# Optimization experiments

Hardware: AMD Instinct MI355X
Metric: run time of the kernel (lower is better)

## Reference

```python
import jax, jax.numpy as jnp
import numpy as np

B, N, C = 128, 2048, 3
VL, PN = 256, 128  # vector_length, prediction_num
NEG_SLOPE = 0.01   # torch LeakyReLU default
BN_EPS = 1e-5


def _lin(key, fin, fout):
    k1, k2 = jax.random.split(key)
    lim = 1.0 / np.sqrt(fin)
    W = jax.random.uniform(k1, (fin, fout), minval=-lim, maxval=lim, dtype=jnp.float32)
    b = jax.random.uniform(k2, (fout,), minval=-lim, maxval=lim, dtype=jnp.float32)
    return W, b


def setup_inputs() -> dict:
    key = jax.random.key(0)
    ks = jax.random.split(key, 14)
    x = jax.random.normal(ks[0], (B, N, C), dtype=jnp.float32)
    lengths = jnp.maximum(jax.random.randint(ks[1], (B,), 0, N), 1).astype(jnp.int32)
    eps = jax.random.normal(ks[2], (B, VL), dtype=jnp.float32)
    W1, b1 = _lin(ks[3], C, 64)
    W2, b2 = _lin(ks[4], 64, 64)
    W3, b3 = _lin(ks[5], 64, 128)
    W4, b4 = _lin(ks[6], 128, 1024)
    Wf, bf = _lin(ks[7], 1024, 1024)
    Wmu, bmu = _lin(ks[8], 1024, VL)
    Wlv, blv = _lin(ks[9], 1024, VL)
    Wd1, bd1 = _lin(ks[10], VL, 1024)
    Wd2, bd2 = _lin(ks[11], 1024, 1024)
    Wd3, bd3 = _lin(ks[12], 1024, PN * C)
    g1 = jnp.ones((1024,), jnp.float32); be1 = jnp.zeros((1024,), jnp.float32)
    g2 = jnp.ones((1024,), jnp.float32); be2 = jnp.zeros((1024,), jnp.float32)
    return dict(x=x, lengths=lengths, eps=eps,
                W1=W1, b1=b1, W2=W2, b2=b2, W3=W3, b3=b3, W4=W4, b4=b4,
                Wf=Wf, bf=bf, Wmu=Wmu, bmu=bmu, Wlv=Wlv, blv=blv,
                Wd1=Wd1, bd1=bd1, g1=g1, be1=be1,
                Wd2=Wd2, bd2=bd2, g2=g2, be2=be2,
                Wd3=Wd3, bd3=bd3)


def _lrelu(h):
    return jnp.where(h > 0, h, NEG_SLOPE * h)


def _bn(h, g, b):
    # BatchNorm1d in training mode: biased batch stats
    m = h.mean(axis=0)
    v = h.var(axis=0)
    return (h - m) * jax.lax.rsqrt(v + BN_EPS) * g + b


def reference(x, lengths, eps,
              W1, b1, W2, b2, W3, b3, W4, b4,
              Wf, bf, Wmu, bmu, Wlv, blv,
              Wd1, bd1, g1, be1, Wd2, bd2, g2, be2, Wd3, bd3):
    # --- pointnet per-point MLP (batched over padded [B,N,C]) ---
    h = _lrelu(x @ W1 + b1)          # [B,N,64]
    h = _lrelu(h @ W2 + b2)          # [B,N,64]
    h = _lrelu(h @ W3 + b3)          # [B,N,128]
    h = _lrelu(h @ W4 + b4)          # [B,N,1024]
    # masked max over points (ragged -> padded+mask)
    mask = jnp.arange(N)[None, :] < lengths[:, None]   # [B,N]
    h = jnp.where(mask[:, :, None], h, -jnp.inf)
    pooled = jnp.max(h, axis=1)      # [B,1024]
    # --- encoder head ---
    e = _lrelu(pooled @ Wf + bf)
    mu = e @ Wmu + bmu               # [B,VL]
    logvar = e @ Wlv + blv           # [B,VL]
    # --- reparameterize ---
    z = mu + eps * jnp.exp(0.5 * logvar)
    # --- decoder: Linear+BN+LeakyReLU x2, final Linear ---
    d = _lrelu(_bn(z @ Wd1 + bd1, g1, be1))
    d = _lrelu(_bn(d @ Wd2 + bd2, g2, be2))
    y = (d @ Wd3 + bd3).reshape(-1, PN, C)   # [B,PN,C]
    return (y, mu, logvar)
```

## Files before the change

kernel.cpp:

```cpp
#include <hip/hip_runtime.h>
#include <hip/hip_bf16.h>
#include <math.h>

#define NEG_SLOPE 0.01f

typedef short short8 __attribute__((ext_vector_type(8)));
typedef float f32x4 __attribute__((ext_vector_type(4)));

__device__ __forceinline__ float lrelu(float v) { return v > 0.0f ? v : NEG_SLOPE * v; }

__device__ __forceinline__ short f2bf(float f) {
    __hip_bfloat16 h = __float2bfloat16(f);
    return __builtin_bit_cast(short, h);
}

__global__ __launch_bounds__(256) void pack_all(
    const float* __restrict__ W4, const float* __restrict__ Wf,
    const float* __restrict__ Wmu, const float* __restrict__ Wlv,
    const float* __restrict__ Wd1, const float* __restrict__ Wd2,
    const float* __restrict__ Wd3, const float* __restrict__ W2,
    const float* __restrict__ W3,
    short* __restrict__ F4, short* __restrict__ Ff, short* __restrict__ Fmuvl,
    short* __restrict__ Fd1, short* __restrict__ Fd2, short* __restrict__ Fd3,
    short* __restrict__ F2, short* __restrict__ F3)
{
    int bid = blockIdx.x;
    const float* src = nullptr; short* dst = nullptr; int K = 0, N = 0; int muvl = 0;
    if      (bid < 64)   { src = W4;  dst = F4;    K = 128;  N = 1024; }
    else if (bid < 576)  { src = Wf;  dst = Ff;    K = 1024; N = 1024; bid -= 64; }
    else if (bid < 832)  { src = nullptr; dst = Fmuvl; K = 1024; N = 512; muvl = 1; bid -= 576; }
    else if (bid < 960)  { src = Wd1; dst = Fd1;   K = 256;  N = 1024; bid -= 832; }
    else if (bid < 1472) { src = Wd2; dst = Fd2;   K = 1024; N = 1024; bid -= 960; }
    else if (bid < 1664) { src = Wd3; dst = Fd3;   K = 1024; N = 384;  bid -= 1472; }
    else if (bid < 1666) { src = W2;  dst = F2;    K = 64;   N = 64;   bid -= 1664; }
    else                 { src = W3;  dst = F3;    K = 64;   N = 128;  bid -= 1666; }

    const int fragid = bid * 4 + (threadIdx.x >> 6);
    const int lane   = threadIdx.x & 63;
    const int K32    = K >> 5;
    const int t   = fragid / (K32 * 4);
    const int rem = fragid - t * K32 * 4;
    const int ks  = rem >> 2;
    const int n   = rem & 3;
    const int col   = t * 64 + n * 16 + (lane & 15);
    const int kbase = ks * 32 + (lane >> 4) * 8;

    short8 v;
#pragma unroll
    for (int e = 0; e < 8; ++e) {
        float f;
        if (muvl) f = (col < 256) ? Wmu[(size_t)(kbase + e) * 256 + col]
                                  : Wlv[(size_t)(kbase + e) * 256 + col - 256];
        else      f = src[(size_t)(kbase + e) * N + col];
        v[e] = f2bf(f);
    }
    *(short8*)&dst[(size_t)fragid * 512 + lane * 8] = v;
}

__global__ __launch_bounds__(128, 2) void h3_kernel(
    const float* __restrict__ x, const int* __restrict__ lengths,
    const float* __restrict__ W1, const float* __restrict__ b1,
    const float* __restrict__ b2, const float* __restrict__ b3,
    const short* __restrict__ F2, const short* __restrict__ F3,
    short* __restrict__ h3p)
{
    const int tid  = threadIdx.x;
    const int b    = blockIdx.x & 127;
    const int c2   = blockIdx.x >> 7;
    const int lane = tid & 63;
    const int w    = tid >> 6;
    const int g    = c2 * 2 + w;
    const int len  = lengths[b];
    if (g * 64 >= len) return;

    __shared__ short S[16384];
    short* Aw = S + w * 8192;
    const int gid = b * 2048 + g * 64 + lane;

    {
        const float x0 = x[gid * 3 + 0];
        const float x1 = x[gid * 3 + 1];
        const float x2 = x[gid * 3 + 2];
#pragma unroll
        for (int q = 0; q < 8; ++q) {
            short8 pv;
#pragma unroll
            for (int e = 0; e < 8; ++e) {
                int c = q * 8 + e;
                float v = b1[c];
                v = fmaf(x0, W1[c], v);
                v = fmaf(x1, W1[64 + c], v);
                v = fmaf(x2, W1[128 + c], v);
                pv[e] = f2bf(lrelu(v));
            }
            *(short8*)&Aw[lane * 64 + ((q ^ (lane & 7)) * 8)] = pv;
        }
    }

    {
        short8 a2[4][2];
#pragma unroll
        for (int m = 0; m < 4; ++m)
#pragma unroll
            for (int ks = 0; ks < 2; ++ks) {
                int rl = m * 16 + (lane & 15);
                int kch = ks * 4 + (lane >> 4);
                a2[m][ks] = *(const short8*)&Aw[rl * 64 + ((kch ^ (rl & 7)) * 8)];
            }
        short8 b2f[2][4];
#pragma unroll
        for (int ks = 0; ks < 2; ++ks)
#pragma unroll
            for (int n = 0; n < 4; ++n)
                b2f[ks][n] = *(const short8*)&F2[(size_t)(ks * 4 + n) * 512 + lane * 8];

        f32x4 acc2[4][4];
#pragma unroll
        for (int m = 0; m < 4; ++m)
#pragma unroll
            for (int n = 0; n < 4; ++n) acc2[m][n] = 0;
#pragma unroll
        for (int ks = 0; ks < 2; ++ks)
#pragma unroll
            for (int n = 0; n < 4; ++n)
#pragma unroll
                for (int m = 0; m < 4; ++m)
                    acc2[m][n] = __builtin_amdgcn_mfma_f32_16x16x32_bf16(
                        a2[m][ks], b2f[ks][n], acc2[m][n], 0, 0, 0);

#pragma unroll
        for (int n = 0; n < 4; ++n) {
            int col = n * 16 + (lane & 15);
            float bv = b2[col];
            int colch = col >> 3;
#pragma unroll
            for (int m = 0; m < 4; ++m)
#pragma unroll
                for (int r = 0; r < 4; ++r) {
                    int rl = m * 16 + (lane >> 4) * 4 + r;
                    Aw[4096 + rl * 64 + ((colch ^ (rl & 7)) * 8) + (col & 7)] =
                        f2bf(lrelu(acc2[m][n][r] + bv));
                }
        }
    }

    {
        short8 a3[4][2];
#pragma unroll
        for (int m = 0; m < 4; ++m)
#pragma unroll
            for (int ks = 0; ks < 2; ++ks) {
                int rl = m * 16 + (lane & 15);
                int kch = ks * 4 + (lane >> 4);
                a3[m][ks] = *(const short8*)&Aw[4096 + rl * 64 + ((kch ^ (rl & 7)) * 8)];
            }
#pragma unroll
        for (int half = 0; half < 2; ++half) {
            short8 b3f[2][4];
#pragma unroll
            for (int ks = 0; ks < 2; ++ks)
#pragma unroll
                for (int n = 0; n < 4; ++n)
                    b3f[ks][n] = *(const short8*)&F3[(size_t)(half * 8 + ks * 4 + n) * 512 + lane * 8];

            f32x4 acc3[4][4];
#pragma unroll
            for (int m = 0; m < 4; ++m)
#pragma unroll
                for (int n = 0; n < 4; ++n) acc3[m][n] = 0;
#pragma unroll
            for (int ks = 0; ks < 2; ++ks)
#pragma unroll
                for (int n = 0; n < 4; ++n)
#pragma unroll
                    for (int m = 0; m < 4; ++m)
                        acc3[m][n] = __builtin_amdgcn_mfma_f32_16x16x32_bf16(
                            a3[m][ks], b3f[ks][n], acc3[m][n], 0, 0, 0);

#pragma unroll
            for (int n = 0; n < 4; ++n) {
                int col = half * 64 + n * 16 + (lane & 15);
                float bv = b3[col];
                int colch = col >> 3;
#pragma unroll
                for (int m = 0; m < 4; ++m)
#pragma unroll
                    for (int r = 0; r < 4; ++r) {
                        int rl = m * 16 + (lane >> 4) * 4 + r;
                        Aw[rl * 128 + ((colch ^ (rl & 7)) * 8) + (col & 7)] =
                            f2bf(lrelu(acc3[m][n][r] + bv));
                    }
            }
        }
    }

    const size_t obase = ((size_t)(b * 32 + g) * 16) * 512 + lane * 8;
#pragma unroll
    for (int ks = 0; ks < 4; ++ks)
#pragma unroll
        for (int m = 0; m < 4; ++m) {
            int rl = m * 16 + (lane & 15);
            int ch = (ks * 4 + (lane >> 4)) ^ (rl & 7);
            short8 af = *(const short8*)&Aw[rl * 128 + ch * 8];
            *(short8*)&h3p[obase + (size_t)(ks * 4 + m) * 512] = af;
        }
}

__global__ __launch_bounds__(256, 3) void l4_pool_kernel(
    const short* __restrict__ h3p, const int* __restrict__ lengths,
    const short* __restrict__ F4, float* __restrict__ part)
{
    const int tid = threadIdx.x, lane = tid & 63, w = tid >> 6;
    const int b = blockIdx.x, ch = blockIdx.y, rs = blockIdx.z;
    const int len = lengths[b];
    const int live32 = (len + 31) >> 5;
    const int cbeg = rs * 8;
    int cend = cbeg + 8; if (cend > live32) cend = live32;
    if (cbeg >= cend) return;

    __shared__ short L[8192];

    const int t = ch * 4 + w;
    short8 bfr[4][4];
#pragma unroll
    for (int ks = 0; ks < 4; ++ks)
#pragma unroll
        for (int n = 0; n < 4; ++n)
            bfr[ks][n] = *(const short8*)&F4[(size_t)((t * 4 + ks) * 4 + n) * 512 + lane * 8];

    const int cfull = len >> 5;
    float madd[2][4];
#pragma unroll
    for (int m = 0; m < 2; ++m)
#pragma unroll
        for (int rr = 0; rr < 4; ++rr)
            madd[m][rr] = (m * 16 + (lane >> 4) * 4 + rr < (len & 31)) ? 0.0f : -INFINITY;

    f32x4 rmax[4];
#pragma unroll
    for (int n = 0; n < 4; ++n)
#pragma unroll
        for (int rr = 0; rr < 4; ++rr) rmax[n][rr] = -INFINITY;

    const size_t bb = (size_t)b * 32;
    short8 stg[2];
    {
        int c64 = cbeg >> 1, mh = cbeg & 1;
#pragma unroll
        for (int pass = 0; pass < 2; ++pass) {
            int idx = pass * 256 + tid, fi = idx >> 6, li = idx & 63;
            stg[pass] = *(const short8*)&h3p[((bb + c64) * 16 + (fi >> 1) * 4 + mh * 2 + (fi & 1)) * 512 + li * 8];
        }
#pragma unroll
        for (int pass = 0; pass < 2; ++pass)
            *(short8*)&L[(pass * 256 + tid) * 8] = stg[pass];
    }
    __syncthreads();

    for (int c = cbeg; c < cend; ++c) {
        const int p = (c - cbeg) & 1;
        if (c + 1 < cend) {
            int c64 = (c + 1) >> 1, mh = (c + 1) & 1;
#pragma unroll
            for (int pass = 0; pass < 2; ++pass) {
                int idx = pass * 256 + tid, fi = idx >> 6, li = idx & 63;
                stg[pass] = *(const short8*)&h3p[((bb + c64) * 16 + (fi >> 1) * 4 + mh * 2 + (fi & 1)) * 512 + li * 8];
            }
        }

        const short* Lb = L + p * 4096;
        f32x4 acc[2][4];
#pragma unroll
        for (int m = 0; m < 2; ++m)
#pragma unroll
            for (int n = 0; n < 4; ++n) acc[m][n] = 0;
#pragma unroll
        for (int ks = 0; ks < 4; ++ks) {
            short8 a0 = *(const short8*)&Lb[(ks * 2 + 0) * 512 + lane * 8];
            short8 a1 = *(const short8*)&Lb[(ks * 2 + 1) * 512 + lane * 8];
#pragma unroll
            for (int n = 0; n < 4; ++n) {
                acc[0][n] = __builtin_amdgcn_mfma_f32_16x16x32_bf16(a0, bfr[ks][n], acc[0][n], 0, 0, 0);
                acc[1][n] = __builtin_amdgcn_mfma_f32_16x16x32_bf16(a1, bfr[ks][n], acc[1][n], 0, 0, 0);
            }
        }
        if (c < cfull) {
#pragma unroll
            for (int n = 0; n < 4; ++n)
#pragma unroll
                for (int rr = 0; rr < 4; ++rr)
                    rmax[n][rr] = fmaxf(rmax[n][rr], fmaxf(acc[0][n][rr], acc[1][n][rr]));
        } else {
#pragma unroll
            for (int n = 0; n < 4; ++n)
#pragma unroll
                for (int rr = 0; rr < 4; ++rr)
                    rmax[n][rr] = fmaxf(rmax[n][rr],
                        fmaxf(acc[0][n][rr] + madd[0][rr], acc[1][n][rr] + madd[1][rr]));
        }
        __syncthreads();
        if (c + 1 < cend) {
            short* Ln = L + (p ^ 1) * 4096;
#pragma unroll
            for (int pass = 0; pass < 2; ++pass)
                *(short8*)&Ln[(pass * 256 + tid) * 8] = stg[pass];
            __syncthreads();
        }
    }

#pragma unroll
    for (int n = 0; n < 4; ++n) {
        float v = fmaxf(fmaxf(rmax[n][0], rmax[n][1]), fmaxf(rmax[n][2], rmax[n][3]));
        v = fmaxf(v, __shfl_xor(v, 16));
        v = fmaxf(v, __shfl_xor(v, 32));
        if (lane < 16)
            part[((size_t)b * 8 + rs) * 1024 + ch * 256 + w * 64 + n * 16 + lane] = v;
    }
}

__global__ __launch_bounds__(256) void reduce_pool_kernel(
    const float* __restrict__ part, const int* __restrict__ lengths,
    const float* __restrict__ b4, short* __restrict__ pooled)
{
    const int b = blockIdx.x;
    const int nlive = (lengths[b] + 255) >> 8;
    for (int i = threadIdx.x; i < 1024; i += 256) {
        float m = part[((size_t)b * 8 + 0) * 1024 + i];
        for (int j = 1; j < nlive; ++j)
            m = fmaxf(m, part[((size_t)b * 8 + j) * 1024 + i]);
        pooled[(size_t)b * 1024 + i] = f2bf(lrelu(m + b4[i]));
    }
}

template<int K32, int EPI>
__global__ __launch_bounds__(64) void gemm16(
    const short* __restrict__ A, const short* __restrict__ Wfrag,
    const float* __restrict__ bias, const float* __restrict__ bias2,
    float* __restrict__ outF, float* __restrict__ outF2,
    short* __restrict__ outB, int Nout)
{
    const int lane = threadIdx.x;
    const int cbb = blockIdx.x, rh = blockIdx.y;
    const int K = K32 * 32;
    const int t = cbb >> 2, n = cbb & 3;

    short8 bf[K32];
#pragma unroll
    for (int ks = 0; ks < K32; ++ks)
        bf[ks] = *(const short8*)&Wfrag[(size_t)((t * K32 + ks) * 4 + n) * 512 + lane * 8];

    const int arow0 = rh * 32 + (lane & 15);
    const int koff  = (lane >> 4) * 8;
    f32x4 acc[2];
    acc[0] = 0; acc[1] = 0;
#pragma unroll
    for (int ks = 0; ks < K32; ++ks) {
        short8 a0 = *(const short8*)&A[(size_t)arow0 * K + ks * 32 + koff];
        short8 a1 = *(const short8*)&A[(size_t)(arow0 + 16) * K + ks * 32 + koff];
        acc[0] = __builtin_amdgcn_mfma_f32_16x16x32_bf16(a0, bf[ks], acc[0], 0, 0, 0);
        acc[1] = __builtin_amdgcn_mfma_f32_16x16x32_bf16(a1, bf[ks], acc[1], 0, 0, 0);
    }

    const int c0 = cbb * 16;
    const int cl = lane & 15;
    if (EPI == 2) {
        const float* bs = (c0 < 256) ? bias : bias2;
        float* of = (c0 < 256) ? outF : outF2;
        int col = (c0 & 255) + cl;
        float bv = bs[col];
#pragma unroll
        for (int m = 0; m < 2; ++m)
#pragma unroll
            for (int rr = 0; rr < 4; ++rr) {
                int row = rh * 32 + m * 16 + (lane >> 4) * 4 + rr;
                of[(size_t)row * 256 + col] = acc[m][rr] + bv;
            }
    } else {
        int col = c0 + cl;
        float bv = bias[col];
#pragma unroll
        for (int m = 0; m < 2; ++m)
#pragma unroll
            for (int rr = 0; rr < 4; ++rr) {
                int row = rh * 32 + m * 16 + (lane >> 4) * 4 + rr;
                float v = acc[m][rr] + bv;
                if (EPI == 1) outB[(size_t)row * Nout + col] = f2bf(lrelu(v));
                else          outF[(size_t)row * Nout + col] = v;
            }
    }
}

template<int K32, bool ZIN>
__global__ __launch_bounds__(256) void gemmBN(
    const short* __restrict__ A, const float* __restrict__ muv,
    const float* __restrict__ lvv, const float* __restrict__ eps,
    const short* __restrict__ Wfrag,
    const float* __restrict__ g, const float* __restrict__ be,
    short* __restrict__ outB, int Nout)
{
    __shared__ float bns[4][16];
    __shared__ float bnq[4][16];

    const int tid = threadIdx.x, lane = tid & 63, w = tid >> 6;
    const int cbb = blockIdx.x;
    const int K = K32 * 32;
    const int t = cbb >> 2, n = cbb & 3;

    short8 bf[K32];
#pragma unroll
    for (int ks = 0; ks < K32; ++ks)
        bf[ks] = *(const short8*)&Wfrag[(size_t)((t * K32 + ks) * 4 + n) * 512 + lane * 8];

    const int arow0 = w * 32 + (lane & 15);
    const int koff  = (lane >> 4) * 8;
    f32x4 acc[2];
    acc[0] = 0; acc[1] = 0;
#pragma unroll
    for (int ks = 0; ks < K32; ++ks) {
        short8 a0, a1;
        if (ZIN) {
#pragma unroll
            for (int e = 0; e < 8; ++e) {
                int k = ks * 32 + koff + e;
                size_t i0 = (size_t)arow0 * 256 + k;
                size_t i1 = (size_t)(arow0 + 16) * 256 + k;
                a0[e] = f2bf(fmaf(eps[i0], expf(0.5f * lvv[i0]), muv[i0]));
                a1[e] = f2bf(fmaf(eps[i1], expf(0.5f * lvv[i1]), muv[i1]));
            }
        } else {
            a0 = *(const short8*)&A[(size_t)arow0 * K + ks * 32 + koff];
            a1 = *(const short8*)&A[(size_t)(arow0 + 16) * K + ks * 32 + koff];
        }
        acc[0] = __builtin_amdgcn_mfma_f32_16x16x32_bf16(a0, bf[ks], acc[0], 0, 0, 0);
        acc[1] = __builtin_amdgcn_mfma_f32_16x16x32_bf16(a1, bf[ks], acc[1], 0, 0, 0);
    }

    float s = 0.f, q = 0.f;
#pragma unroll
    for (int m = 0; m < 2; ++m)
#pragma unroll
        for (int rr = 0; rr < 4; ++rr) {
            float v = acc[m][rr];
            s += v; q = fmaf(v, v, q);
        }
    s += __shfl_xor(s, 16); s += __shfl_xor(s, 32);
    q += __shfl_xor(q, 16); q += __shfl_xor(q, 32);
    if (lane < 16) { bns[w][lane] = s; bnq[w][lane] = q; }
    __syncthreads();

    const int cl = lane & 15;
    float st = bns[0][cl] + bns[1][cl] + bns[2][cl] + bns[3][cl];
    float qt = bnq[0][cl] + bnq[1][cl] + bnq[2][cl] + bnq[3][cl];
    float mean = st * (1.0f / 128.0f);
    float var  = qt * (1.0f / 128.0f) - mean * mean;
    float rs   = 1.0f / sqrtf(var + 1e-5f);
    const int col = cbb * 16 + cl;
    float gg = g[col] * rs;
    float bb = be[col] - mean * gg;

#pragma unroll
    for (int m = 0; m < 2; ++m)
#pragma unroll
        for (int rr = 0; rr < 4; ++rr) {
            int row = w * 32 + m * 16 + (lane >> 4) * 4 + rr;
            outB[(size_t)row * Nout + col] = f2bf(lrelu(fmaf(acc[m][rr], gg, bb)));
        }
}

extern "C" void kernel_launch(void* const* d_in, const int* in_sizes, int n_in,
                              void* d_out, int out_size, void* d_ws, size_t ws_size,
                              hipStream_t stream)
{
    const float* x       = (const float*)d_in[0];
    const int*   lengths = (const int*)  d_in[1];
    const float* eps     = (const float*)d_in[2];
    const float* W1  = (const float*)d_in[3];  const float* b1  = (const float*)d_in[4];
    const float* W2  = (const float*)d_in[5];  const float* b2  = (const float*)d_in[6];
    const float* W3  = (const float*)d_in[7];  const float* b3  = (const float*)d_in[8];
    const float* W4  = (const float*)d_in[9];  const float* b4  = (const float*)d_in[10];
    const float* Wf  = (const float*)d_in[11]; const float* bf  = (const float*)d_in[12];
    const float* Wmu = (const float*)d_in[13]; const float* bmu = (const float*)d_in[14];
    const float* Wlv = (const float*)d_in[15]; const float* blv = (const float*)d_in[16];
    const float* Wd1 = (const float*)d_in[17];
    const float* g1  = (const float*)d_in[19]; const float* be1 = (const float*)d_in[20];
    const float* Wd2 = (const float*)d_in[21];
    const float* g2  = (const float*)d_in[23]; const float* be2 = (const float*)d_in[24];
    const float* Wd3 = (const float*)d_in[25]; const float* bd3 = (const float*)d_in[26];

    float* out = (float*)d_out;
    float* y_out  = out;
    float* mu_out = out + 49152;
    float* lv_out = out + 81920;

    char* ws = (char*)d_ws;
    short* F4    = (short*)(ws + 0);
    short* Ff    = (short*)(ws + 262144);
    short* Fmuvl = (short*)(ws + 2359296);
    short* Fd1   = (short*)(ws + 3407872);
    short* Fd2   = (short*)(ws + 3932160);
    short* Fd3   = (short*)(ws + 6029312);
    short* F2    = (short*)(ws + 6815744);
    short* F3    = (short*)(ws + 6823936);
    short* h3p   = (short*)(ws + 6840320);
    float* part  = (float*)(ws + 73949184);
    short* pooled = (short*)(ws + 6840320 + 0);
    short* ebuf   = (short*)(ws + 6840320 + 262144);
    short* d1v    = (short*)(ws + 6840320 + 524288);
    short* d2v    = (short*)(ws + 6840320 + 786432);

    pack_all<<<1670, 256, 0, stream>>>(W4, Wf, Wmu, Wlv, Wd1, Wd2, Wd3, W2, W3,
                                       F4, Ff, Fmuvl, Fd1, Fd2, Fd3, F2, F3);
    h3_kernel<<<2048, 128, 0, stream>>>(x, lengths, W1, b1, b2, b3, F2, F3, h3p);
    l4_pool_kernel<<<dim3(128, 4, 8), 256, 0, stream>>>(h3p, lengths, F4, part);
    reduce_pool_kernel<<<128, 256, 0, stream>>>(part, lengths, b4, pooled);
    gemm16<32, 1><<<dim3(64, 4), 64, 0, stream>>>(pooled, Ff, bf, nullptr,
                                                  nullptr, nullptr, ebuf, 1024);
    gemm16<32, 2><<<dim3(32, 4), 64, 0, stream>>>(ebuf, Fmuvl, bmu, blv,
                                                  mu_out, lv_out, nullptr, 256);
    gemmBN<8, true><<<64, 256, 0, stream>>>(nullptr, mu_out, lv_out, eps,
                                            Fd1, g1, be1, d1v, 1024);
    gemmBN<32, false><<<64, 256, 0, stream>>>(d1v, nullptr, nullptr, nullptr,
                                              Fd2, g2, be2, d2v, 1024);
    gemm16<32, 0><<<dim3(24, 4), 64, 0, stream>>>(d2v, Fd3, bd3, nullptr,
                                                  y_out, nullptr, nullptr, 384);
}
```

Measured before the change: 121.3 us.

## Process 64-point chunks per iteration in layer-4 pool with single barrier

The layer-4 matmul plus masked-max kernel now stages a full 64-row chunk (16 fragments) into a doubled LDS buffer per iteration instead of a 32-row half-chunk. This halves the number of loop iterations and the contiguous global loads become simpler. The staging write into the alternate buffer is moved before one shared barrier, removing the second __syncthreads per iteration. Masking now applies only on the last partial chunk. The cost is twice the LDS footprint, which may reduce occupancy, and more staging registers.

```diff
diff --git a/kernel.cpp b/kernel.cpp
--- a/kernel.cpp
+++ b/kernel.cpp
@@ -213,12 +213,12 @@
     const int tid = threadIdx.x, lane = tid & 63, w = tid >> 6;
     const int b = blockIdx.x, ch = blockIdx.y, rs = blockIdx.z;
     const int len = lengths[b];
-    const int live32 = (len + 31) >> 5;
-    const int cbeg = rs * 8;
-    int cend = cbeg + 8; if (cend > live32) cend = live32;
+    const int live64 = (len + 63) >> 6;
+    const int cbeg = rs * 4;
+    int cend = cbeg + 4; if (cend > live64) cend = live64;
     if (cbeg >= cend) return;
 
-    __shared__ short L[8192];
+    __shared__ short L[16384];
 
     const int t = ch * 4 + w;
     short8 bfr[4][4];
@@ -228,13 +228,8 @@
         for (int n = 0; n < 4; ++n)
             bfr[ks][n] = *(const short8*)&F4[(size_t)((t * 4 + ks) * 4 + n) * 512 + lane * 8];
 
-    const int cfull = len >> 5;
-    float madd[2][4];
-#pragma unroll
-    for (int m = 0; m < 2; ++m)
-#pragma unroll
-        for (int rr = 0; rr < 4; ++rr)
-            madd[m][rr] = (m * 16 + (lane >> 4) * 4 + rr < (len & 31)) ? 0.0f : -INFINITY;
+    const int partial = (len & 63) ? (live64 - 1) : -1;
+    const int rem = len & 63;
 
     f32x4 rmax[4];
 #pragma unroll
@@ -243,16 +238,14 @@
         for (int rr = 0; rr < 4; ++rr) rmax[n][rr] = -INFINITY;
 
     const size_t bb = (size_t)b * 32;
-    short8 stg[2];
+    short8 stg[4];
     {
-        int c64 = cbeg >> 1, mh = cbeg & 1;
-#pragma unroll
-        for (int pass = 0; pass < 2; ++pass) {
-            int idx = pass * 256 + tid, fi = idx >> 6, li = idx & 63;
-            stg[pass] = *(const short8*)&h3p[((bb + c64) * 16 + (fi >> 1) * 4 + mh * 2 + (fi & 1)) * 512 + li * 8];
-        }
-#pragma unroll
-        for (int pass = 0; pass < 2; ++pass)
+        const size_t fb = (bb + cbeg) * 16 * 512;
+#pragma unroll
+        for (int pass = 0; pass < 4; ++pass)
+            stg[pass] = *(const short8*)&h3p[fb + (size_t)(pass * 256 + tid) * 8];
+#pragma unroll
+        for (int pass = 0; pass < 4; ++pass)
             *(short8*)&L[(pass * 256 + tid) * 8] = stg[pass];
     }
     __syncthreads();
@@ -260,52 +253,59 @@
     for (int c = cbeg; c < cend; ++c) {
         const int p = (c - cbeg) & 1;
         if (c + 1 < cend) {
-            int c64 = (c + 1) >> 1, mh = (c + 1) & 1;
-#pragma unroll
-            for (int pass = 0; pass < 2; ++pass) {
-                int idx = pass * 256 + tid, fi = idx >> 6, li = idx & 63;
-                stg[pass] = *(const short8*)&h3p[((bb + c64) * 16 + (fi >> 1) * 4 + mh * 2 + (fi & 1)) * 512 + li * 8];
-            }
-        }
-
-        const short* Lb = L + p * 4096;
-        f32x4 acc[2][4];
-#pragma unroll
-        for (int m = 0; m < 2; ++m)
-#pragma unroll
-            for (int n = 0; n < 4; ++n) acc[m][n] = 0;
-#pragma unroll
-        for (int ks = 0; ks < 4; ++ks) {
-            short8 a0 = *(const short8*)&Lb[(ks * 2 + 0) * 512 + lane * 8];
-            short8 a1 = *(const short8*)&Lb[(ks * 2 + 1) * 512 + lane * 8];
-#pragma unroll
-            for (int n = 0; n < 4; ++n) {
-                acc[0][n] = __builtin_amdgcn_mfma_f32_16x16x32_bf16(a0, bfr[ks][n], acc[0][n], 0, 0, 0);
-                acc[1][n] = __builtin_amdgcn_mfma_f32_16x16x32_bf16(a1, bfr[ks][n], acc[1][n], 0, 0, 0);
-            }
-        }
-        if (c < cfull) {
-#pragma unroll
-            for (int n = 0; n < 4; ++n)
-#pragma unroll
-                for (int rr = 0; rr < 4; ++rr)
-                    rmax[n][rr] = fmaxf(rmax[n][rr], fmaxf(acc[0][n][rr], acc[1][n][rr]));
-        } else {
-#pragma unroll
-            for (int n = 0; n < 4; ++n)
-#pragma unroll
-                for (int rr = 0; rr < 4; ++rr)
-                    rmax[n][rr] = fmaxf(rmax[n][rr],
-                        fmaxf(acc[0][n][rr] + madd[0][rr], acc[1][n][rr] + madd[1][rr]));
+            const size_t fb = (bb + c + 1) * 16 * 512;
+#pragma unroll
+            for (int pass = 0; pass < 4; ++pass)
+                stg[pass] = *(const short8*)&h3p[fb + (size_t)(pass * 256 + tid) * 8];
+        }
+
+        const short* Lb = L + p * 8192;
+#pragma unroll
+        for (int mh = 0; mh < 2; ++mh) {
+            f32x4 acc[2][4];
+#pragma unroll
+            for (int j = 0; j < 2; ++j)
+#pragma unroll
+                for (int n = 0; n < 4; ++n) acc[j][n] = 0;
+#pragma unroll
+            for (int ks = 0; ks < 4; ++ks) {
+                short8 a0 = *(const short8*)&Lb[(ks * 4 + mh * 2 + 0) * 512 + lane * 8];
+                short8 a1 = *(const short8*)&Lb[(ks * 4 + mh * 2 + 1) * 512 + lane * 8];
+#pragma unroll
+                for (int n = 0; n < 4; ++n) {
+                    acc[0][n] = __builtin_amdgcn_mfma_f32_16x16x32_bf16(a0, bfr[ks][n], acc[0][n], 0, 0, 0);
+                    acc[1][n] = __builtin_amdgcn_mfma_f32_16x16x32_bf16(a1, bfr[ks][n], acc[1][n], 0, 0, 0);
+                }
+            }
+            if (c == partial) {
+#pragma unroll
+                for (int j = 0; j < 2; ++j)
+#pragma unroll
+                    for (int n = 0; n < 4; ++n)
+#pragma unroll
+                        for (int rr = 0; rr < 4; ++rr) {
+                            int row = mh * 32 + j * 16 + (lane >> 4) * 4 + rr;
+                            rmax[n][rr] = fmaxf(rmax[n][rr],
+                                (row < rem) ? acc[j][n][rr] : -INFINITY);
+                        }
+            } else {
+#pragma unroll
+                for (int j = 0; j < 2; ++j)
+#pragma unroll
+                    for (int n = 0; n < 4; ++n)
+#pragma unroll
+                        for (int rr = 0; rr < 4; ++rr)
+                            rmax[n][rr] = fmaxf(rmax[n][rr], acc[j][n][rr]);
+            }
+        }
+
+        if (c + 1 < cend) {
+            short* Ln = L + (p ^ 1) * 8192;
+#pragma unroll
+            for (int pass = 0; pass < 4; ++pass)
+                *(short8*)&Ln[(pass * 256 + tid) * 8] = stg[pass];
         }
         __syncthreads();
-        if (c + 1 < cend) {
-            short* Ln = L + (p ^ 1) * 4096;
-#pragma unroll
-            for (int pass = 0; pass < 2; ++pass)
-                *(short8*)&Ln[(pass * 256 + tid) * 8] = stg[pass];
-            __syncthreads();
-        }
     }
 
 #pragma unroll
```

Result: no change. 120.2 us (-0.9%).

## Widen l4_pool channel tile per wave to halve h3 staging reloads

Applied to the files above, without the earlier changes.

Each wave now holds 8 column tiles of W4 (128 channels) in registers instead of 4, so the grid's channel dimension shrinks from 4 to 2 and each staged h3 chunk in LDS is reused across twice as many output channels. The MFMA loop is restructured to process one 16-row half at a time with 8 accumulators, and the double-buffer synchronisation is simplified to a single barrier per iteration. This cuts global and LDS traffic for h3p. In exchange it raises register pressure (twice the B fragments and running maxima), and the occupancy hint of 3 is dropped, which may reduce occupancy.

```diff
diff --git a/kernel.cpp b/kernel.cpp
--- a/kernel.cpp
+++ b/kernel.cpp
@@ -206,12 +206,12 @@
         }
 }
 
-__global__ __launch_bounds__(256, 3) void l4_pool_kernel(
+__global__ __launch_bounds__(256) void l4_pool_kernel(
     const short* __restrict__ h3p, const int* __restrict__ lengths,
     const short* __restrict__ F4, float* __restrict__ part)
 {
     const int tid = threadIdx.x, lane = tid & 63, w = tid >> 6;
-    const int b = blockIdx.x, ch = blockIdx.y, rs = blockIdx.z;
+    const int b = blockIdx.x, rs = blockIdx.y, ch = blockIdx.z;
     const int len = lengths[b];
     const int live32 = (len + 31) >> 5;
     const int cbeg = rs * 8;
@@ -220,13 +220,15 @@
 
     __shared__ short L[8192];
 
-    const int t = ch * 4 + w;
-    short8 bfr[4][4];
+    short8 bfr[4][8];
 #pragma unroll
     for (int ks = 0; ks < 4; ++ks)
 #pragma unroll
-        for (int n = 0; n < 4; ++n)
-            bfr[ks][n] = *(const short8*)&F4[(size_t)((t * 4 + ks) * 4 + n) * 512 + lane * 8];
+        for (int n = 0; n < 8; ++n) {
+            int tt = ch * 8 + w * 2 + (n >> 2);
+            bfr[ks][n] = *(const short8*)&F4[
+                (size_t)((tt * 4 + ks) * 4 + (n & 3)) * 512 + lane * 8];
+        }
 
     const int cfull = len >> 5;
     float madd[2][4];
@@ -236,20 +238,21 @@
         for (int rr = 0; rr < 4; ++rr)
             madd[m][rr] = (m * 16 + (lane >> 4) * 4 + rr < (len & 31)) ? 0.0f : -INFINITY;
 
-    f32x4 rmax[4];
-#pragma unroll
-    for (int n = 0; n < 4; ++n)
+    f32x4 rmax[8];
+#pragma unroll
+    for (int n = 0; n < 8; ++n)
 #pragma unroll
         for (int rr = 0; rr < 4; ++rr) rmax[n][rr] = -INFINITY;
 
     const size_t bb = (size_t)b * 32;
     short8 stg[2];
     {
-        int c64 = cbeg >> 1, mh = cbeg & 1;
+        int g_ = cbeg >> 1, h_ = cbeg & 1;
 #pragma unroll
         for (int pass = 0; pass < 2; ++pass) {
             int idx = pass * 256 + tid, fi = idx >> 6, li = idx & 63;
-            stg[pass] = *(const short8*)&h3p[((bb + c64) * 16 + (fi >> 1) * 4 + mh * 2 + (fi & 1)) * 512 + li * 8];
+            stg[pass] = *(const short8*)&h3p[
+                ((bb + g_) * 16 + (fi >> 1) * 4 + h_ * 2 + (fi & 1)) * 512 + li * 8];
         }
 #pragma unroll
         for (int pass = 0; pass < 2; ++pass)
@@ -258,63 +261,63 @@
     __syncthreads();
 
     for (int c = cbeg; c < cend; ++c) {
-        const int p = (c - cbeg) & 1;
+        const int p2 = (c - cbeg) & 1;
         if (c + 1 < cend) {
-            int c64 = (c + 1) >> 1, mh = (c + 1) & 1;
+            int g_ = (c + 1) >> 1, h_ = (c + 1) & 1;
 #pragma unroll
             for (int pass = 0; pass < 2; ++pass) {
                 int idx = pass * 256 + tid, fi = idx >> 6, li = idx & 63;
-                stg[pass] = *(const short8*)&h3p[((bb + c64) * 16 + (fi >> 1) * 4 + mh * 2 + (fi & 1)) * 512 + li * 8];
-            }
-        }
-
-        const short* Lb = L + p * 4096;
-        f32x4 acc[2][4];
-#pragma unroll
-        for (int m = 0; m < 2; ++m)
-#pragma unroll
-            for (int n = 0; n < 4; ++n) acc[m][n] = 0;
-#pragma unroll
-        for (int ks = 0; ks < 4; ++ks) {
-            short8 a0 = *(const short8*)&Lb[(ks * 2 + 0) * 512 + lane * 8];
-            short8 a1 = *(const short8*)&Lb[(ks * 2 + 1) * 512 + lane * 8];
-#pragma unroll
-            for (int n = 0; n < 4; ++n) {
-                acc[0][n] = __builtin_amdgcn_mfma_f32_16x16x32_bf16(a0, bfr[ks][n], acc[0][n], 0, 0, 0);
-                acc[1][n] = __builtin_amdgcn_mfma_f32_16x16x32_bf16(a1, bfr[ks][n], acc[1][n], 0, 0, 0);
-            }
-        }
-        if (c < cfull) {
-#pragma unroll
-            for (int n = 0; n < 4; ++n)
-#pragma unroll
-                for (int rr = 0; rr < 4; ++rr)
-                    rmax[n][rr] = fmaxf(rmax[n][rr], fmaxf(acc[0][n][rr], acc[1][n][rr]));
-        } else {
-#pragma unroll
-            for (int n = 0; n < 4; ++n)
-#pragma unroll
-                for (int rr = 0; rr < 4; ++rr)
-                    rmax[n][rr] = fmaxf(rmax[n][rr],
-                        fmaxf(acc[0][n][rr] + madd[0][rr], acc[1][n][rr] + madd[1][rr]));
-        }
-        __syncthreads();
+                stg[pass] = *(const short8*)&h3p[
+                    ((bb + g_) * 16 + (fi >> 1) * 4 + h_ * 2 + (fi & 1)) * 512 + li * 8];
+            }
+        }
+
+        const short* Lb = L + p2 * 4096;
+#pragma unroll
+        for (int j = 0; j < 2; ++j) {
+            f32x4 acc[8];
+#pragma unroll
+            for (int n = 0; n < 8; ++n) acc[n] = 0;
+#pragma unroll
+            for (int ks = 0; ks < 4; ++ks) {
+                short8 a = *(const short8*)&Lb[(ks * 2 + j) * 512 + lane * 8];
+#pragma unroll
+                for (int n = 0; n < 8; ++n)
+                    acc[n] = __builtin_amdgcn_mfma_f32_16x16x32_bf16(
+                        a, bfr[ks][n], acc[n], 0, 0, 0);
+            }
+            if (c < cfull) {
+#pragma unroll
+                for (int n = 0; n < 8; ++n)
+#pragma unroll
+                    for (int rr = 0; rr < 4; ++rr)
+                        rmax[n][rr] = fmaxf(rmax[n][rr], acc[n][rr]);
+            } else {
+#pragma unroll
+                for (int n = 0; n < 8; ++n)
+#pragma unroll
+                    for (int rr = 0; rr < 4; ++rr)
+                        rmax[n][rr] = fmaxf(rmax[n][rr], acc[n][rr] + madd[j][rr]);
+            }
+        }
+
         if (c + 1 < cend) {
-            short* Ln = L + (p ^ 1) * 4096;
+            short* Ln = L + (p2 ^ 1) * 4096;
 #pragma unroll
             for (int pass = 0; pass < 2; ++pass)
                 *(short8*)&Ln[(pass * 256 + tid) * 8] = stg[pass];
-            __syncthreads();
-        }
-    }
-
-#pragma unroll
-    for (int n = 0; n < 4; ++n) {
-        float v = fmaxf(fmaxf(rmax[n][0], rmax[n][1]), fmaxf(rmax[n][2], rmax[n][3]));
+        }
+        __syncthreads();
+    }
+
+#pragma unroll
+    for (int n = 0; n < 8; ++n) {
+        float v = fmaxf(fmaxf(rmax[n][0], rmax[n][1]),
+                        fmaxf(rmax[n][2], rmax[n][3]));
         v = fmaxf(v, __shfl_xor(v, 16));
         v = fmaxf(v, __shfl_xor(v, 32));
         if (lane < 16)
-            part[((size_t)b * 8 + rs) * 1024 + ch * 256 + w * 64 + n * 16 + lane] = v;
+            part[((size_t)b * 8 + rs) * 1024 + ch * 512 + w * 128 + n * 16 + lane] = v;
     }
 }
 
@@ -511,7 +514,7 @@
     pack_all<<<1670, 256, 0, stream>>>(W4, Wf, Wmu, Wlv, Wd1, Wd2, Wd3, W2, W3,
                                        F4, Ff, Fmuvl, Fd1, Fd2, Fd3, F2, F3);
     h3_kernel<<<2048, 128, 0, stream>>>(x, lengths, W1, b1, b2, b3, F2, F3, h3p);
-    l4_pool_kernel<<<dim3(128, 4, 8), 256, 0, stream>>>(h3p, lengths, F4, part);
+    l4_pool_kernel<<<dim3(128, 8, 2), 256, 0, stream>>>(h3p, lengths, F4, part);
     reduce_pool_kernel<<<128, 256, 0, stream>>>(part, lengths, b4, pooled);
     gemm16<32, 1><<<dim3(64, 4), 64, 0, stream>>>(pooled, Ff, bf, nullptr,
                                                   nullptr, nullptr, ebuf, 1024);
```

Measured after the change: 167.2 us. +37.8%, slower.
